# Kernel optimization log

Measured on AMD Instinct MI355X. Metric: run time of the kernel, lower is better.

## Reference

```python
import jax, jax.numpy as jnp
import numpy as np

VOCAB = 38
EMB = 128
CTX = 5  # context window size
HIDDEN = [512, 256, 128]


def setup_inputs() -> dict:
    key = jax.random.key(0)
    ks = jax.random.split(key, 16)
    B, S = 64, 1024
    encrypted_input = jax.random.randint(ks[0], (B, S), 0, VOCAB, dtype=jnp.int32)
    # embedding table, uniform(-0.1, 0.1), padding_idx=0 row zeroed
    emb = jax.random.uniform(ks[1], (VOCAB, EMB), jnp.float32, -0.1, 0.1)
    emb = emb.at[0].set(0.0)
    dims = [EMB * CTX] + HIDDEN + [VOCAB]
    params = {}
    for i in range(len(dims) - 1):
        fan_in, fan_out = dims[i], dims[i + 1]
        limit = float(np.sqrt(6.0 / (fan_in + fan_out)))  # xavier uniform
        params[f"W{i+1}"] = jax.random.uniform(ks[2 + i], (fan_out, fan_in), jnp.float32, -limit, limit)
        params[f"b{i+1}"] = jnp.zeros((fan_out,), jnp.float32)
    return {"encrypted_input": encrypted_input, "emb": emb, **params}


def reference(encrypted_input, emb, W1, b1, W2, b2, W3, b3, W4, b4):
    B, S = encrypted_input.shape
    pad = CTX // 2
    x = emb[encrypted_input]                                   # [B, S, E]
    xp = jnp.pad(x, ((0, 0), (pad, pad), (0, 0)))              # [B, S+4, E]
    # sliding window of CTX tokens, flattened -> [B, S, CTX*E]
    ctx = jnp.concatenate([xp[:, i:i + S, :] for i in range(CTX)], axis=-1)
    h = ctx.reshape(B * S, CTX * EMB)                          # fused batched GEMM rows
    h = jax.nn.relu(h @ W1.T + b1)
    h = jax.nn.relu(h @ W2.T + b2)
    h = jax.nn.relu(h @ W3.T + b3)
    out = h @ W4.T + b4                                        # [B*S, VOCAB]
    return out.reshape(B, S, VOCAB)
```

## Files before the change

### kernel.cpp

```cpp
#include <hip/hip_runtime.h>
#include <hip/hip_bf16.h>

#define SEQ 1024

typedef __attribute__((ext_vector_type(8))) short s16x8;
typedef __attribute__((ext_vector_type(4))) float f32x4;
typedef __attribute__((ext_vector_type(2))) unsigned int u32x2;
typedef __attribute__((ext_vector_type(4))) unsigned int u32x4;
typedef __attribute__((ext_vector_type(2))) float f32x2;

#define GT  0
#define W2P (5 * 39 * 512)
#define W3P (W2P + 16 * 16 * 512)
#define W4P (W3P + 8 * 8 * 512)

#define F2 (16 * 16)
#define F3 (8 * 8)
#define F4 (3 * 4)
#define FTOT (F2 + F3 + F4)
#define GC_BLOCKS 195

__device__ __forceinline__ unsigned int f2bf(float f) {
    unsigned int u = __float_as_uint(f);
    return (u + 0x7fffu + ((u >> 16) & 1u)) >> 16;
}

__device__ __forceinline__ unsigned short bfbits(float f) {
    __hip_bfloat16 h = __float2bfloat16(f);
    unsigned short u;
    __builtin_memcpy(&u, &h, 2);
    return u;
}

__device__ __forceinline__ unsigned pk2(float a, float b) {
    return (unsigned)bfbits(a) | ((unsigned)bfbits(b) << 16);
}

__global__ void prep_kernel(const float* __restrict__ w1, const float* __restrict__ w2,
                            const float* __restrict__ w3, const float* __restrict__ w4,
                            const float* __restrict__ emb, unsigned short* __restrict__ dst) {
    if (blockIdx.x < GC_BLOCKS) {
        const int j = blockIdx.x / 39;
        const int v = blockIdx.x % 39;
        const int o = threadIdx.x;
        if (v >= 38) {
            dst[GT + (j * 39 + v) * 512 + o] = 0;
            return;
        }
        __shared__ float ev[128];
        if (threadIdx.x < 128) ev[threadIdx.x] = emb[v * 128 + threadIdx.x];
        __syncthreads();
        const float* wr = w1 + o * 640 + j * 128;
        float s = 0.f;
        #pragma unroll
        for (int e = 0; e < 128; e += 4) {
            const float4 a = *reinterpret_cast<const float4*>(wr + e);
            s += a.x * ev[e] + a.y * ev[e + 1] + a.z * ev[e + 2] + a.w * ev[e + 3];
        }
        dst[GT + (j * 39 + v) * 512 + o] = bfbits(s);
    } else {
        const int g = (blockIdx.x - GC_BLOCKS) * 512 + threadIdx.x;
        if (g >= FTOT * 64) return;
        const int lane = g & 63;
        const int t    = g >> 6;
        const float* w; int K, N, KC, base, tl;
        if (t < F2)           { w = w2; K = 512; N = 256; KC = 16; base = W2P; tl = t; }
        else if (t < F2 + F3) { w = w3; K = 256; N = 128; KC = 8;  base = W3P; tl = t - F2; }
        else                  { w = w4; K = 128; N = 38;  KC = 4;  base = W4P; tl = t - F2 - F3; }
        const int ct  = tl / KC;
        const int kc  = tl - ct * KC;
        const int col = ct * 16 + (lane & 15);
        const int k0  = kc * 32 + (lane >> 4) * 8;
        unsigned short o8[8];
        #pragma unroll
        for (int e = 0; e < 8; ++e)
            o8[e] = (col < N) ? (unsigned short)f2bf(w[col * K + k0 + e]) : (unsigned short)0;
        *reinterpret_cast<s16x8*>(dst + base + (size_t)(tl * 64 + lane) * 8) =
            *reinterpret_cast<s16x8*>(o8);
    }
}

#define H1S 0
#define H2S 65536
#define H3S 0

#define SWZ(b, row) ((b) ^ (((row) & 15) << 4))

__device__ __forceinline__ u32x2 pack_relu(f32x4 a, float4 b) {
    u32x2 r;
    r[0] = pk2(fmaxf(a[0] + b.x, 0.f), fmaxf(a[1] + b.y, 0.f));
    r[1] = pk2(fmaxf(a[2] + b.z, 0.f), fmaxf(a[3] + b.w, 0.f));
    return r;
}

__launch_bounds__(1024, 4)
__global__ void fused_mlp(const int* __restrict__ tok,
                          const unsigned short* __restrict__ wbf,
                          const float* __restrict__ b1,
                          const float* __restrict__ b2,
                          const float* __restrict__ b3,
                          const float* __restrict__ b4,
                          float* __restrict__ out) {
    __shared__ char smem[98304];
    const int tid  = threadIdx.x;
    const int lane = tid & 63;
    const int wave = tid >> 6;
    const int l15  = lane & 15;
    const int l4   = lane >> 4;
    const int r0   = blockIdx.x * 64;
    const int s0   = r0 & (SEQ - 1);
    const int bat  = r0 >> 10;

    int* tokLDS = reinterpret_cast<int*>(smem + H2S);

    if (tid < 68) {
        const int sp = s0 - 2 + tid;
        tokLDS[tid] = (sp >= 0 && sp < SEQ) ? tok[bat * SEQ + sp] : 38;
    }
    __syncthreads();

    {
        const unsigned short* gt = wbf + GT;
        #pragma unroll
        for (int it = 0; it < 4; ++it) {
            const int item = it * 1024 + tid;
            const int row  = item >> 6;
            const int c    = item & 63;
            float s[8];
            {
                const float4 blo = *reinterpret_cast<const float4*>(b1 + c * 8);
                const float4 bhi = *reinterpret_cast<const float4*>(b1 + c * 8 + 4);
                s[0] = blo.x; s[1] = blo.y; s[2] = blo.z; s[3] = blo.w;
                s[4] = bhi.x; s[5] = bhi.y; s[6] = bhi.z; s[7] = bhi.w;
            }
            #pragma unroll
            for (int j = 0; j < 5; ++j) {
                const int t = tokLDS[row + j];
                const s16x8 g = *reinterpret_cast<const s16x8*>(gt + (j * 39 + t) * 512 + c * 8);
                #pragma unroll
                for (int e = 0; e < 8; ++e)
                    s[e] += __uint_as_float(((unsigned)(unsigned short)g[e]) << 16);
            }
            u32x4 wv;
            #pragma unroll
            for (int h = 0; h < 4; ++h)
                wv[h] = pk2(fmaxf(s[2 * h], 0.f), fmaxf(s[2 * h + 1], 0.f));
            *reinterpret_cast<u32x4*>(smem + H1S + SWZ(row * 1024 + c * 16, row)) = wv;
        }
    }
    __syncthreads();

    {
        f32x4 acc[4];
        #pragma unroll
        for (int n = 0; n < 4; ++n) acc[n] = (f32x4){0.f, 0.f, 0.f, 0.f};
        for (int ks = 0; ks < 16; ++ks) {
            s16x8 xv[4];
            #pragma unroll
            for (int n = 0; n < 4; ++n) {
                const int row = n * 16 + l15;
                xv[n] = *reinterpret_cast<const s16x8*>(
                    smem + H1S + SWZ(row * 1024 + ks * 64 + l4 * 16, row));
            }
            s16x8 w = *reinterpret_cast<const s16x8*>(
                wbf + W2P + ((wave * 16 + ks) * 64 + lane) * 8);
            #pragma unroll
            for (int n = 0; n < 4; ++n)
                acc[n] = __builtin_amdgcn_mfma_f32_16x16x32_bf16(w, xv[n], acc[n], 0, 0, 0);
        }
        const int col0 = wave * 16 + l4 * 4;
        const float4 bb = *reinterpret_cast<const float4*>(b2 + col0);
        #pragma unroll
        for (int n = 0; n < 4; ++n) {
            const int row = n * 16 + l15;
            *reinterpret_cast<u32x2*>(smem + H2S + SWZ(row * 512 + col0 * 2, row)) =
                pack_relu(acc[n], bb);
        }
    }
    __syncthreads();

    {
        const int ct = wave & 7;
        const int nh = wave >> 3;
        f32x4 acc[2];
        #pragma unroll
        for (int i = 0; i < 2; ++i) acc[i] = (f32x4){0.f, 0.f, 0.f, 0.f};
        for (int ks = 0; ks < 8; ++ks) {
            s16x8 w = *reinterpret_cast<const s16x8*>(
                wbf + W3P + ((ct * 8 + ks) * 64 + lane) * 8);
            #pragma unroll
            for (int i = 0; i < 2; ++i) {
                const int row = (nh * 2 + i) * 16 + l15;
                s16x8 xv = *reinterpret_cast<const s16x8*>(
                    smem + H2S + SWZ(row * 512 + ks * 64 + l4 * 16, row));
                acc[i] = __builtin_amdgcn_mfma_f32_16x16x32_bf16(w, xv, acc[i], 0, 0, 0);
            }
        }
        const int col0 = ct * 16 + l4 * 4;
        const float4 bb = *reinterpret_cast<const float4*>(b3 + col0);
        #pragma unroll
        for (int i = 0; i < 2; ++i) {
            const int row = (nh * 2 + i) * 16 + l15;
            *reinterpret_cast<u32x2*>(smem + H3S + SWZ(row * 256 + col0 * 2, row)) =
                pack_relu(acc[i], bb);
        }
    }
    __syncthreads();

    if (wave < 12) {
        const int mt = wave >> 2;
        const int n  = wave & 3;
        f32x4 acc = (f32x4){0.f, 0.f, 0.f, 0.f};
        #pragma unroll
        for (int ks = 0; ks < 4; ++ks) {
            const int row = n * 16 + l15;
            s16x8 xv = *reinterpret_cast<const s16x8*>(
                smem + H3S + SWZ(row * 256 + ks * 64 + l4 * 16, row));
            s16x8 w = *reinterpret_cast<const s16x8*>(
                wbf + W4P + ((mt * 4 + ks) * 64 + lane) * 8);
            acc = __builtin_amdgcn_mfma_f32_16x16x32_bf16(w, xv, acc, 0, 0, 0);
        }
        const int rg   = r0 + n * 16 + l15;
        const int col0 = mt * 16 + l4 * 4;
        #pragma unroll
        for (int h = 0; h < 2; ++h) {
            const int c = col0 + 2 * h;
            if (c < 38) {
                f32x2 v;
                v[0] = acc[2 * h]     + b4[c];
                v[1] = acc[2 * h + 1] + b4[c + 1];
                *reinterpret_cast<f32x2*>(out + rg * 38 + c) = v;
            }
        }
    }
}

extern "C" void kernel_launch(void* const* d_in, const int* in_sizes, int n_in,
                              void* d_out, int out_size, void* d_ws, size_t ws_size,
                              hipStream_t stream) {
    const int*   tok = (const int*)d_in[0];
    const float* emb = (const float*)d_in[1];
    const float* W1  = (const float*)d_in[2];
    const float* b1  = (const float*)d_in[3];
    const float* W2  = (const float*)d_in[4];
    const float* b2  = (const float*)d_in[5];
    const float* W3  = (const float*)d_in[6];
    const float* b3  = (const float*)d_in[7];
    const float* W4  = (const float*)d_in[8];
    const float* b4  = (const float*)d_in[9];
    float* out = (float*)d_out;
    unsigned short* wbf = (unsigned short*)d_ws;

    const int pack_blocks = (FTOT * 64 + 511) / 512;
    prep_kernel<<<GC_BLOCKS + pack_blocks, 512, 0, stream>>>(W1, W2, W3, W4, emb, wbf);
    fused_mlp<<<1024, 1024, 0, stream>>>(tok, wbf, b1, b2, b3, b4, out);
}
```

Baseline: 54.19 us.

## Precombine token-pair layer-1 tables and shrink blocks to 32 rows

Layer-1 contributions are now precomputed as pair tables (positions 0+1 with bias folded in, and 3+4), plus a single table for position 2, in a new prep2 kernel. The fused kernel then gathers three vectors per row instead of five plus bias. The block tile also drops from 64 rows and 1024 threads to 32 rows and 512 threads with half the LDS, giving 2048 blocks and more resident blocks per CU. The cost is an extra prep launch and about 3 MB of pair tables written each call, with fewer rows sharing each weight load.

```diff
diff --git a/kernel.cpp b/kernel.cpp
--- a/kernel.cpp
+++ b/kernel.cpp
@@ -9,16 +9,18 @@
 typedef __attribute__((ext_vector_type(4))) unsigned int u32x4;
 typedef __attribute__((ext_vector_type(2))) float f32x2;
 
-#define GT  0
-#define W2P (5 * 39 * 512)
-#define W3P (W2P + 16 * 16 * 512)
-#define W4P (W3P + 8 * 8 * 512)
+#define P01P 0
+#define G2P  (1521 * 512)
+#define P34P (G2P + 39 * 512)
+#define W2P  (P34P + 1521 * 512)
+#define W3P  (W2P + 256 * 512)
+#define W4P  (W3P + 64 * 512)
+#define BF_END (W4P + 12 * 512)
 
 #define F2 (16 * 16)
 #define F3 (8 * 8)
 #define F4 (3 * 4)
 #define FTOT (F2 + F3 + F4)
-#define GC_BLOCKS 195
 
 __device__ __forceinline__ unsigned int f2bf(float f) {
     unsigned int u = __float_as_uint(f);
@@ -36,17 +38,19 @@
     return (unsigned)bfbits(a) | ((unsigned)bfbits(b) << 16);
 }
 
-__global__ void prep_kernel(const float* __restrict__ w1, const float* __restrict__ w2,
-                            const float* __restrict__ w3, const float* __restrict__ w4,
-                            const float* __restrict__ emb, unsigned short* __restrict__ dst) {
-    if (blockIdx.x < GC_BLOCKS) {
+__device__ __forceinline__ float bf2f(short x) {
+    return __uint_as_float(((unsigned)(unsigned short)x) << 16);
+}
+
+__global__ void prep1(const float* __restrict__ w1, const float* __restrict__ w2,
+                      const float* __restrict__ w3, const float* __restrict__ w4,
+                      const float* __restrict__ emb, unsigned short* __restrict__ dst) {
+    if (blockIdx.x < 195) {
+        float* gf = reinterpret_cast<float*>(dst + BF_END);
         const int j = blockIdx.x / 39;
         const int v = blockIdx.x % 39;
         const int o = threadIdx.x;
-        if (v >= 38) {
-            dst[GT + (j * 39 + v) * 512 + o] = 0;
-            return;
-        }
+        if (v >= 38) { gf[(j * 39 + v) * 512 + o] = 0.f; return; }
         __shared__ float ev[128];
         if (threadIdx.x < 128) ev[threadIdx.x] = emb[v * 128 + threadIdx.x];
         __syncthreads();
@@ -57,9 +61,9 @@
             const float4 a = *reinterpret_cast<const float4*>(wr + e);
             s += a.x * ev[e] + a.y * ev[e + 1] + a.z * ev[e + 2] + a.w * ev[e + 3];
         }
-        dst[GT + (j * 39 + v) * 512 + o] = bfbits(s);
+        gf[(j * 39 + v) * 512 + o] = s;
     } else {
-        const int g = (blockIdx.x - GC_BLOCKS) * 512 + threadIdx.x;
+        const int g = (blockIdx.x - 195) * 512 + threadIdx.x;
         if (g >= FTOT * 64) return;
         const int lane = g & 63;
         const int t    = g >> 6;
@@ -80,8 +84,26 @@
     }
 }
 
+__global__ void prep2(const float* __restrict__ b1, unsigned short* __restrict__ dst) {
+    const float* gf = reinterpret_cast<const float*>(dst + BF_END);
+    const int o   = threadIdx.x;
+    const int bid = blockIdx.x;
+    if (bid < 1521) {
+        const int v0 = bid / 39, v1 = bid % 39;
+        const float s = b1[o] + gf[(0 * 39 + v0) * 512 + o] + gf[(1 * 39 + v1) * 512 + o];
+        dst[P01P + bid * 512 + o] = bfbits(s);
+    } else if (bid < 1560) {
+        const int v = bid - 1521;
+        dst[G2P + v * 512 + o] = bfbits(gf[(2 * 39 + v) * 512 + o]);
+    } else {
+        const int p = bid - 1560;
+        const int v3 = p / 39, v4 = p % 39;
+        dst[P34P + p * 512 + o] = bfbits(gf[(3 * 39 + v3) * 512 + o] + gf[(4 * 39 + v4) * 512 + o]);
+    }
+}
+
 #define H1S 0
-#define H2S 65536
+#define H2S 32768
 #define H3S 0
 
 #define SWZ(b, row) ((b) ^ (((row) & 15) << 4))
@@ -93,134 +115,134 @@
     return r;
 }
 
-__launch_bounds__(1024, 4)
+__launch_bounds__(512, 6)
 __global__ void fused_mlp(const int* __restrict__ tok,
                           const unsigned short* __restrict__ wbf,
-                          const float* __restrict__ b1,
                           const float* __restrict__ b2,
                           const float* __restrict__ b3,
                           const float* __restrict__ b4,
                           float* __restrict__ out) {
-    __shared__ char smem[98304];
+    __shared__ char smem[49152];
     const int tid  = threadIdx.x;
     const int lane = tid & 63;
     const int wave = tid >> 6;
     const int l15  = lane & 15;
     const int l4   = lane >> 4;
-    const int r0   = blockIdx.x * 64;
+    const int r0   = blockIdx.x * 32;
     const int s0   = r0 & (SEQ - 1);
     const int bat  = r0 >> 10;
 
-    int* tokLDS = reinterpret_cast<int*>(smem + H2S);
-
-    if (tid < 68) {
+    int* tokL = reinterpret_cast<int*>(smem + H2S);
+
+    if (tid < 36) {
         const int sp = s0 - 2 + tid;
-        tokLDS[tid] = (sp >= 0 && sp < SEQ) ? tok[bat * SEQ + sp] : 38;
+        tokL[tid] = (sp >= 0 && sp < SEQ) ? tok[bat * SEQ + sp] : 38;
     }
     __syncthreads();
 
     {
-        const unsigned short* gt = wbf + GT;
+        const int row = tid >> 4;
+        const int c16 = tid & 15;
+        const int t0 = tokL[row],     t1 = tokL[row + 1], t2 = tokL[row + 2];
+        const int t3 = tokL[row + 3], t4 = tokL[row + 4];
+        const unsigned short* pa = wbf + P01P + (t0 * 39 + t1) * 512;
+        const unsigned short* pb = wbf + G2P  + t2 * 512;
+        const unsigned short* pc = wbf + P34P + (t3 * 39 + t4) * 512;
         #pragma unroll
         for (int it = 0; it < 4; ++it) {
-            const int item = it * 1024 + tid;
-            const int row  = item >> 6;
-            const int c    = item & 63;
-            float s[8];
-            {
-                const float4 blo = *reinterpret_cast<const float4*>(b1 + c * 8);
-                const float4 bhi = *reinterpret_cast<const float4*>(b1 + c * 8 + 4);
-                s[0] = blo.x; s[1] = blo.y; s[2] = blo.z; s[3] = blo.w;
-                s[4] = bhi.x; s[5] = bhi.y; s[6] = bhi.z; s[7] = bhi.w;
-            }
-            #pragma unroll
-            for (int j = 0; j < 5; ++j) {
-                const int t = tokLDS[row + j];
-                const s16x8 g = *reinterpret_cast<const s16x8*>(gt + (j * 39 + t) * 512 + c * 8);
+            const int c8 = it * 16 + c16;
+            const s16x8 va = *reinterpret_cast<const s16x8*>(pa + c8 * 8);
+            const s16x8 vb = *reinterpret_cast<const s16x8*>(pb + c8 * 8);
+            const s16x8 vc = *reinterpret_cast<const s16x8*>(pc + c8 * 8);
+            u32x4 wv;
+            #pragma unroll
+            for (int h = 0; h < 4; ++h) {
+                const float e0 = bf2f(va[2 * h])     + bf2f(vb[2 * h])     + bf2f(vc[2 * h]);
+                const float e1 = bf2f(va[2 * h + 1]) + bf2f(vb[2 * h + 1]) + bf2f(vc[2 * h + 1]);
+                wv[h] = pk2(fmaxf(e0, 0.f), fmaxf(e1, 0.f));
+            }
+            *reinterpret_cast<u32x4*>(smem + H1S + SWZ(row * 1024 + c8 * 16, row)) = wv;
+        }
+    }
+    __syncthreads();
+
+    {
+        f32x4 acc[2][2];
+        #pragma unroll
+        for (int rt = 0; rt < 2; ++rt)
+            #pragma unroll
+            for (int ct = 0; ct < 2; ++ct) acc[rt][ct] = (f32x4){0.f, 0.f, 0.f, 0.f};
+        for (int ks = 0; ks < 16; ++ks) {
+            s16x8 xv[2];
+            #pragma unroll
+            for (int rt = 0; rt < 2; ++rt) {
+                const int row = rt * 16 + l15;
+                xv[rt] = *reinterpret_cast<const s16x8*>(
+                    smem + H1S + SWZ(row * 1024 + ks * 64 + l4 * 16, row));
+            }
+            #pragma unroll
+            for (int ct = 0; ct < 2; ++ct) {
+                const s16x8 w = *reinterpret_cast<const s16x8*>(
+                    wbf + W2P + (((wave * 2 + ct) * 16 + ks) * 64 + lane) * 8);
                 #pragma unroll
-                for (int e = 0; e < 8; ++e)
-                    s[e] += __uint_as_float(((unsigned)(unsigned short)g[e]) << 16);
-            }
-            u32x4 wv;
-            #pragma unroll
-            for (int h = 0; h < 4; ++h)
-                wv[h] = pk2(fmaxf(s[2 * h], 0.f), fmaxf(s[2 * h + 1], 0.f));
-            *reinterpret_cast<u32x4*>(smem + H1S + SWZ(row * 1024 + c * 16, row)) = wv;
+                for (int rt = 0; rt < 2; ++rt)
+                    acc[rt][ct] = __builtin_amdgcn_mfma_f32_16x16x32_bf16(w, xv[rt], acc[rt][ct], 0, 0, 0);
+            }
+        }
+        #pragma unroll
+        for (int ct = 0; ct < 2; ++ct) {
+            const int col0 = (wave * 2 + ct) * 16 + l4 * 4;
+            const float4 bb = *reinterpret_cast<const float4*>(b2 + col0);
+            #pragma unroll
+            for (int rt = 0; rt < 2; ++rt) {
+                const int row = rt * 16 + l15;
+                *reinterpret_cast<u32x2*>(smem + H2S + SWZ(row * 512 + col0 * 2, row)) =
+                    pack_relu(acc[rt][ct], bb);
+            }
         }
     }
     __syncthreads();
 
     {
-        f32x4 acc[4];
-        #pragma unroll
-        for (int n = 0; n < 4; ++n) acc[n] = (f32x4){0.f, 0.f, 0.f, 0.f};
-        for (int ks = 0; ks < 16; ++ks) {
-            s16x8 xv[4];
-            #pragma unroll
-            for (int n = 0; n < 4; ++n) {
-                const int row = n * 16 + l15;
-                xv[n] = *reinterpret_cast<const s16x8*>(
-                    smem + H1S + SWZ(row * 1024 + ks * 64 + l4 * 16, row));
-            }
-            s16x8 w = *reinterpret_cast<const s16x8*>(
-                wbf + W2P + ((wave * 16 + ks) * 64 + lane) * 8);
-            #pragma unroll
-            for (int n = 0; n < 4; ++n)
-                acc[n] = __builtin_amdgcn_mfma_f32_16x16x32_bf16(w, xv[n], acc[n], 0, 0, 0);
+        f32x4 acc[2];
+        #pragma unroll
+        for (int rt = 0; rt < 2; ++rt) acc[rt] = (f32x4){0.f, 0.f, 0.f, 0.f};
+        for (int ks = 0; ks < 8; ++ks) {
+            const s16x8 w = *reinterpret_cast<const s16x8*>(
+                wbf + W3P + ((wave * 8 + ks) * 64 + lane) * 8);
+            #pragma unroll
+            for (int rt = 0; rt < 2; ++rt) {
+                const int row = rt * 16 + l15;
+                const s16x8 xv = *reinterpret_cast<const s16x8*>(
+                    smem + H2S + SWZ(row * 512 + ks * 64 + l4 * 16, row));
+                acc[rt] = __builtin_amdgcn_mfma_f32_16x16x32_bf16(w, xv, acc[rt], 0, 0, 0);
+            }
         }
         const int col0 = wave * 16 + l4 * 4;
-        const float4 bb = *reinterpret_cast<const float4*>(b2 + col0);
-        #pragma unroll
-        for (int n = 0; n < 4; ++n) {
-            const int row = n * 16 + l15;
-            *reinterpret_cast<u32x2*>(smem + H2S + SWZ(row * 512 + col0 * 2, row)) =
-                pack_relu(acc[n], bb);
-        }
-    }
-    __syncthreads();
-
-    {
-        const int ct = wave & 7;
-        const int nh = wave >> 3;
-        f32x4 acc[2];
-        #pragma unroll
-        for (int i = 0; i < 2; ++i) acc[i] = (f32x4){0.f, 0.f, 0.f, 0.f};
-        for (int ks = 0; ks < 8; ++ks) {
-            s16x8 w = *reinterpret_cast<const s16x8*>(
-                wbf + W3P + ((ct * 8 + ks) * 64 + lane) * 8);
-            #pragma unroll
-            for (int i = 0; i < 2; ++i) {
-                const int row = (nh * 2 + i) * 16 + l15;
-                s16x8 xv = *reinterpret_cast<const s16x8*>(
-                    smem + H2S + SWZ(row * 512 + ks * 64 + l4 * 16, row));
-                acc[i] = __builtin_amdgcn_mfma_f32_16x16x32_bf16(w, xv, acc[i], 0, 0, 0);
-            }
-        }
-        const int col0 = ct * 16 + l4 * 4;
         const float4 bb = *reinterpret_cast<const float4*>(b3 + col0);
         #pragma unroll
-        for (int i = 0; i < 2; ++i) {
-            const int row = (nh * 2 + i) * 16 + l15;
+        for (int rt = 0; rt < 2; ++rt) {
+            const int row = rt * 16 + l15;
             *reinterpret_cast<u32x2*>(smem + H3S + SWZ(row * 256 + col0 * 2, row)) =
-                pack_relu(acc[i], bb);
-        }
-    }
-    __syncthreads();
-
-    if (wave < 12) {
-        const int mt = wave >> 2;
-        const int n  = wave & 3;
+                pack_relu(acc[rt], bb);
+        }
+    }
+    __syncthreads();
+
+    if (wave < 6) {
+        const int rt = wave & 1;
+        const int mt = wave >> 1;
         f32x4 acc = (f32x4){0.f, 0.f, 0.f, 0.f};
         #pragma unroll
         for (int ks = 0; ks < 4; ++ks) {
-            const int row = n * 16 + l15;
-            s16x8 xv = *reinterpret_cast<const s16x8*>(
+            const int row = rt * 16 + l15;
+            const s16x8 xv = *reinterpret_cast<const s16x8*>(
                 smem + H3S + SWZ(row * 256 + ks * 64 + l4 * 16, row));
-            s16x8 w = *reinterpret_cast<const s16x8*>(
+            const s16x8 w = *reinterpret_cast<const s16x8*>(
                 wbf + W4P + ((mt * 4 + ks) * 64 + lane) * 8);
             acc = __builtin_amdgcn_mfma_f32_16x16x32_bf16(w, xv, acc, 0, 0, 0);
         }
-        const int rg   = r0 + n * 16 + l15;
+        const int rg   = r0 + rt * 16 + l15;
         const int col0 = mt * 16 + l4 * 4;
         #pragma unroll
         for (int h = 0; h < 2; ++h) {
@@ -252,6 +274,7 @@
     unsigned short* wbf = (unsigned short*)d_ws;
 
     const int pack_blocks = (FTOT * 64 + 511) / 512;
-    prep_kernel<<<GC_BLOCKS + pack_blocks, 512, 0, stream>>>(W1, W2, W3, W4, emb, wbf);
-    fused_mlp<<<1024, 1024, 0, stream>>>(tok, wbf, b1, b2, b3, b4, out);
-}
+    prep1<<<195 + pack_blocks, 512, 0, stream>>>(W1, W2, W3, W4, emb, wbf);
+    prep2<<<1521 + 39 + 1521, 512, 0, stream>>>(b1, wbf);
+    fused_mlp<<<2048, 512, 0, stream>>>(tok, wbf, b2, b3, b4, out);
+}
```

Measured after the change: 60.59 us. 11.8% more time.
